# Performance work log

Hardware: AMD Instinct MI355X
Metric: run time of the kernel (lower is better)

Reference implementation:

```python
import jax, jax.numpy as jnp
import numpy as np

B, N, D, K, L, NC = 8, 4096, 64, 8, 2, 2
EPS = 1e-5


def setup_inputs() -> dict:
    key = jax.random.key(0)
    ks = iter(jax.random.split(key, 64))
    def p(*shape, s=0.05):
        return jax.random.normal(next(ks), shape, dtype=jnp.float32) * s
    return dict(
        x=p(B, N, 3, s=1.0),
        ew1=p(3, D), eb1=jnp.zeros((D,), jnp.float32), ew2=p(D, D), eb2=jnp.zeros((D,), jnp.float32),
        wq=p(L, D, D), bq=jnp.zeros((L, D), jnp.float32), wk=p(L, D, D), bk=jnp.zeros((L, D), jnp.float32),
        wv=p(L, D, D), bv=jnp.zeros((L, D), jnp.float32),
        pw1=p(L, 3, D), pb1=jnp.zeros((L, D), jnp.float32), pw2=p(L, D, D), pb2=jnp.zeros((L, D), jnp.float32),
        aw=p(L, D), ab=jnp.zeros((L,), jnp.float32),
        ow=p(L, D, D), ob=jnp.zeros((L, D), jnp.float32),
        l1g=jnp.ones((L, D), jnp.float32), l1b=jnp.zeros((L, D), jnp.float32),
        l2g=jnp.ones((L, D), jnp.float32), l2b=jnp.zeros((L, D), jnp.float32),
        fw1=p(L, D, 2 * D), fb1=jnp.zeros((L, 2 * D), jnp.float32),
        fw2=p(L, 2 * D, D), fb2=jnp.zeros((L, D), jnp.float32),
        cw=p(D, 2 * D), cb=jnp.zeros((2 * D,), jnp.float32),
        cg=jnp.ones((2 * D,), jnp.float32), cbeta=jnp.zeros((2 * D,), jnp.float32),
        f1w=p(2 * D, 128), f1b=jnp.zeros((128,), jnp.float32),
        b1g=jnp.ones((128,), jnp.float32), b1b=jnp.zeros((128,), jnp.float32),
        f2w=p(128, 64), f2b=jnp.zeros((64,), jnp.float32),
        b2g=jnp.ones((64,), jnp.float32), b2b=jnp.zeros((64,), jnp.float32),
        f3w=p(64, NC), f3b=jnp.zeros((NC,), jnp.float32),
    )


def _ln(x, g, b):
    m = jnp.mean(x, -1, keepdims=True)
    v = jnp.mean((x - m) ** 2, -1, keepdims=True)
    return g * (x - m) * jax.lax.rsqrt(v + EPS) + b


def _bn(x, g, b):
    # eval-mode BatchNorm with running_mean=0, running_var=1
    return g * x * jax.lax.rsqrt(jnp.float32(1.0 + EPS)) + b


def _knn(pos, k):
    sq = jnp.sum(pos * pos, -1)  # [B,N]
    d2 = sq[:, :, None] - 2.0 * jnp.einsum('bnd,bmd->bnm', pos, pos) + sq[:, None, :]
    _, idx = jax.lax.top_k(-d2, k)  # k smallest distances (includes self)
    return jax.lax.stop_gradient(idx)  # [B,N,k]


def _gather(t, idx):
    b, n, k = idx.shape
    flat = idx.reshape(b, n * k)
    return jnp.take_along_axis(t, flat[:, :, None], axis=1).reshape(b, n, k, t.shape[-1])


def _block(x, pos, idx, pr):
    (wq, bq, wk, bk, wv, bv, pw1, pb1, pw2, pb2, aw, ab,
     ow, ob, l1g, l1b, l2g, l2b, fw1, fb1, fw2, fb2) = pr
    q = x @ wq + bq
    k = x @ wk + bk
    v = x @ wv + bv
    kg = _gather(k, idx)      # [B,N,K,C]
    vg = _gather(v, idx)
    pg = _gather(pos, idx)    # [B,N,K,3]
    pd = pos[:, :, None, :] - pg
    pe = jax.nn.relu(pd @ pw1 + pb1) @ pw2 + pb2
    ai = q[:, :, None, :] - kg + pe  # subtraction attention
    logits = jnp.einsum('bnkc,c->bnk', ai, aw) + ab
    w = jax.nn.softmax(logits, axis=-1)
    out = jnp.einsum('bnk,bnkc->bnc', w, vg + pe)
    out = out @ ow + ob
    out = _ln(out + x, l1g, l1b)
    ffn = jax.nn.gelu(out @ fw1 + fb1, approximate=False) @ fw2 + fb2
    return _ln(out + ffn, l2g, l2b)


def reference(x, ew1, eb1, ew2, eb2, wq, bq, wk, bk, wv, bv, pw1, pb1, pw2, pb2,
              aw, ab, ow, ob, l1g, l1b, l2g, l2b, fw1, fb1, fw2, fb2,
              cw, cb, cg, cbeta, f1w, f1b, b1g, b1b, f2w, f2b, b2g, b2b, f3w, f3b):
    pos = x
    h = jax.nn.relu(x @ ew1 + eb1) @ ew2 + eb2  # [B,N,D]
    idx = _knn(pos, K)
    stacked = (wq, bq, wk, bk, wv, bv, pw1, pb1, pw2, pb2, aw, ab,
               ow, ob, l1g, l1b, l2g, l2b, fw1, fb1, fw2, fb2)
    for i in range(L):
        h = _block(h, pos, idx, tuple(a[i] for a in stacked))
    y = jax.nn.relu(_bn(h @ cw + cb, cg, cbeta))  # [B,N,2D]
    g = jnp.max(y, axis=1)  # global max pool over points
    g = jax.nn.relu(_bn(g @ f1w + f1b, b1g, b1b))
    g = jax.nn.relu(_bn(g @ f2w + f2b, b2g, b2b))
    return g @ f3w + f3b  # [B, NC]
```

## Files before the change

### kernel.cpp

```cpp
#include <hip/hip_runtime.h>
#include <cmath>

#define BB 8
#define NN 4096
#define DD 64
#define KK 8
#define NCLS 2

constexpr float LNEPS = 1e-5f;
constexpr float BNRS = 0.9999950000374994f;
constexpr float INVSQRT2 = 0.70710678118654752440f;

#define QPB 64
#define SPLITS 16
#define SUBSET 64

__device__ __forceinline__ float wave_sum(float v) {
#pragma unroll
  for (int m = 32; m > 0; m >>= 1) v += __shfl_xor(v, m, 64);
  return v;
}

__device__ __forceinline__ float gelu_exact(float x) {
  return 0.5f * x * (1.0f + erff(x * INVSQRT2));
}

__device__ __forceinline__ float dist2(float4 q, float4 p) {
  float dot = fmaf(q.x, p.x, fmaf(q.y, p.y, q.z * p.z));
  return fmaf(-2.0f, dot, q.w + p.w);
}

__global__ void zero_kernel(float* g) { g[threadIdx.x] = 0.0f; }

__global__ __launch_bounds__(256) void embed_kernel(
    const float* __restrict__ x, const float* __restrict__ ew1, const float* __restrict__ eb1,
    const float* __restrict__ ew2, const float* __restrict__ eb2, float* __restrict__ h) {
  __shared__ float h1[4][DD];
  int w = threadIdx.x >> 6, c = threadIdx.x & 63;
  int pt = ((blockIdx.x & 7) << 12) + (blockIdx.x >> 3) * 4 + w;
  const float* xp = x + (size_t)pt * 3;
  float x0 = xp[0], x1 = xp[1], x2 = xp[2];
  float a = fmaf(x0, ew1[c], fmaf(x1, ew1[64 + c], fmaf(x2, ew1[128 + c], eb1[c])));
  h1[w][c] = fmaxf(a, 0.0f);
  float s = eb2[c];
#pragma unroll 8
  for (int d = 0; d < DD; d++) s = fmaf(h1[w][d], ew2[d * 64 + c], s);
  h[(size_t)pt * 64 + c] = s;
}

__global__ __launch_bounds__(256) void knn_prep_kernel(const float* __restrict__ x,
                                                       float4* __restrict__ ppg) {
  int i = ((blockIdx.x & 7) << 12) + (blockIdx.x >> 3) * 256 + threadIdx.x;
  float a0 = x[3 * i + 0], a1 = x[3 * i + 1], a2 = x[3 * i + 2];
  ppg[i] = make_float4(a0, a1, a2, a0 * a0 + a1 * a1 + a2 * a2);
}

__global__ __launch_bounds__(1024) void knn_kernel(const float4* __restrict__ ppg,
                                                   int* __restrict__ idx) {
  __shared__ union {
    float v[SPLITS * 8][QPB];
    double k[SPLITS * 8][QPB];
  } mb;
  __shared__ float thrq[QPB];
  int b = blockIdx.x & 7;
  int qbase = (blockIdx.x >> 3) * QPB;
  const float4* pb = ppg + (size_t)b * NN;
  int ql = threadIdx.x & 63;
  int sp = __builtin_amdgcn_readfirstlane(threadIdx.x >> 6);
  float4 qp = pb[qbase + ql];
  const float4* cp = pb + sp * (NN / SPLITS);

  float bd[8];
#pragma unroll
  for (int u = 0; u < 8; u++) bd[u] = INFINITY;
#pragma unroll 4
  for (int jj = 0; jj < SUBSET; ++jj) {
    float d2 = dist2(qp, cp[jj]);
#pragma unroll
    for (int u = 7; u > 0; --u) bd[u] = fminf(bd[u], fmaxf(bd[u - 1], d2));
    bd[0] = fminf(bd[0], d2);
  }
#pragma unroll
  for (int u = 0; u < 8; u++) mb.v[sp * 8 + u][ql] = bd[u];
  __syncthreads();

  if (sp < 8) {
    float cd[8];
#pragma unroll
    for (int u = 0; u < 8; u++) cd[u] = INFINITY;
    int base = sp * 16;
#pragma unroll
    for (int e = 0; e < 16; e++) {
      float vv = mb.v[base + e][ql];
#pragma unroll
      for (int u = 7; u > 0; --u) cd[u] = fminf(cd[u], fmaxf(cd[u - 1], vv));
      cd[0] = fminf(cd[0], vv);
    }
#pragma unroll
    for (int u = 0; u < 8; u++) mb.v[base + u][ql] = cd[u];
  }
  __syncthreads();

  if (sp == 0) {
    float cd[8];
#pragma unroll
    for (int u = 0; u < 8; u++) cd[u] = INFINITY;
    for (int m = 0; m < 8; m++) {
      for (int e = 0; e < 8; e++) {
        float vv = mb.v[m * 16 + e][ql];
        if (__all(vv >= cd[7])) break;
#pragma unroll
        for (int u = 7; u > 0; --u) cd[u] = fminf(cd[u], fmaxf(cd[u - 1], vv));
        cd[0] = fminf(cd[0], vv);
      }
    }
    thrq[ql] = cd[7];
  }
  __syncthreads();
  float U = thrq[ql];

  double kd[8];
#pragma unroll
  for (int u = 0; u < 8; u++) kd[u] = INFINITY;
#pragma unroll 4
  for (int jj = 0; jj < NN / SPLITS; ++jj) {
    float d2 = dist2(qp, cp[jj]);
    if (d2 <= U) {
      double key = __hiloint2double(__float_as_int(d2), sp * (NN / SPLITS) + jj);
      if (key < kd[7]) {
#pragma unroll
        for (int u = 7; u > 0; --u) kd[u] = fmin(kd[u], fmax(kd[u - 1], key));
        kd[0] = fmin(kd[0], key);
      }
    }
  }
#pragma unroll
  for (int u = 0; u < 8; u++) mb.k[sp * 8 + u][ql] = kd[u];
  __syncthreads();

  if (sp < 8) {
    double cd[8];
#pragma unroll
    for (int u = 0; u < 8; u++) cd[u] = INFINITY;
    int base = sp * 16;
#pragma unroll
    for (int e = 0; e < 16; e++) {
      double key = mb.k[base + e][ql];
#pragma unroll
      for (int u = 7; u > 0; --u) cd[u] = fmin(cd[u], fmax(cd[u - 1], key));
      cd[0] = fmin(cd[0], key);
    }
#pragma unroll
    for (int u = 0; u < 8; u++) mb.k[base + u][ql] = cd[u];
  }
  __syncthreads();

  if (sp == 0) {
    double cd[8];
#pragma unroll
    for (int u = 0; u < 8; u++) cd[u] = INFINITY;
    for (int m = 0; m < 8; m++) {
      for (int e = 0; e < 8; e++) {
        double key = mb.k[m * 16 + e][ql];
        if (__all(key >= cd[7])) break;
#pragma unroll
        for (int u = 7; u > 0; --u) cd[u] = fmin(cd[u], fmax(cd[u - 1], key));
        cd[0] = fmin(cd[0], key);
      }
    }
    int* op = idx + ((size_t)b * NN + qbase + ql) * 8;
#pragma unroll
    for (int u = 0; u < 8; u++) op[u] = __double2loint(cd[u]);
  }
}

__global__ __launch_bounds__(64) void qkv_kernel(
    const float* __restrict__ h, const float* __restrict__ wq, const float* __restrict__ bq,
    const float* __restrict__ wk, const float* __restrict__ bk,
    const float* __restrict__ wv, const float* __restrict__ bv,
    float* __restrict__ q, float* __restrict__ k, float* __restrict__ v) {
  __shared__ __attribute__((aligned(16))) float hb[DD][4];
  int c = threadIdx.x;
  int b = blockIdx.x & 7, pos = blockIdx.x >> 3;
  int p0 = (b << 12) + pos * 4;
#pragma unroll
  for (int i = 0; i < 4; i++) hb[c][i] = h[(size_t)(p0 + i) * 64 + c];
  float bqc = bq[c], bkc = bk[c], bvc = bv[c];
  float aq[4], ak[4], av[4];
#pragma unroll
  for (int i = 0; i < 4; i++) { aq[i] = bqc; ak[i] = bkc; av[i] = bvc; }
#pragma unroll 4
  for (int d = 0; d < DD; d++) {
    float wq_ = wq[d * 64 + c], wk_ = wk[d * 64 + c], wv_ = wv[d * 64 + c];
    float4 hh = *(const float4*)&hb[d][0];
    aq[0] = fmaf(hh.x, wq_, aq[0]); aq[1] = fmaf(hh.y, wq_, aq[1]);
    aq[2] = fmaf(hh.z, wq_, aq[2]); aq[3] = fmaf(hh.w, wq_, aq[3]);
    ak[0] = fmaf(hh.x, wk_, ak[0]); ak[1] = fmaf(hh.y, wk_, ak[1]);
    ak[2] = fmaf(hh.z, wk_, ak[2]); ak[3] = fmaf(hh.w, wk_, ak[3]);
    av[0] = fmaf(hh.x, wv_, av[0]); av[1] = fmaf(hh.y, wv_, av[1]);
    av[2] = fmaf(hh.z, wv_, av[2]); av[3] = fmaf(hh.w, wv_, av[3]);
  }
#pragma unroll
  for (int i = 0; i < 4; i++) {
    q[(size_t)(p0 + i) * 64 + c] = aq[i];
    k[(size_t)(p0 + i) * 64 + c] = ak[i];
    v[(size_t)(p0 + i) * 64 + c] = av[i];
  }
}

__global__ __launch_bounds__(64) void attn_kernel(
    const float* __restrict__ x, const float* __restrict__ h,
    const float* q, const float* __restrict__ kk, const float* __restrict__ vv,
    const int* __restrict__ idx,
    const float* __restrict__ pw1, const float* __restrict__ pb1,
    const float* __restrict__ pw2, const float* __restrict__ pb2,
    const float* __restrict__ aw, const float* __restrict__ ab,
    const float* __restrict__ ow, const float* __restrict__ ob,
    const float* __restrict__ l1g, const float* __restrict__ l1b,
    float* t) {
  __shared__ __attribute__((aligned(16))) float h1b[2][DD][8];
  __shared__ __attribute__((aligned(16))) float outb[2][DD];
  int c = threadIdx.x;
  int b = blockIdx.x & 7;
  int n0 = (blockIdx.x >> 3) * 2;
  int p0 = (b << 12) + n0;
  const float* xb = x + (size_t)b * NN * 3;
  float w1c0 = pw1[c], w1c1 = pw1[64 + c], w1c2 = pw1[128 + c], b1c = pb1[c];
  float pb2c = pb2[c], lawc = aw[c], lobc = ob[c], g1c = l1g[c], bt1c = l1b[c];
  float lab = ab[0];
  float hs0 = h[(size_t)p0 * 64 + c], hs1 = h[(size_t)(p0 + 1) * 64 + c];
  float qs0 = q[(size_t)p0 * 64 + c], qs1 = q[(size_t)(p0 + 1) * 64 + c];
  int nb[2][8];
#pragma unroll
  for (int u = 0; u < 8; u++) {
    nb[0][u] = idx[(size_t)p0 * 8 + u];
    nb[1][u] = idx[(size_t)(p0 + 1) * 8 + u];
  }
  float kv0[8], kv1[8], vg0[8], vg1[8];
#pragma unroll
  for (int u = 0; u < 8; u++) {
    kv0[u] = kk[((size_t)(b << 12) + nb[0][u]) * 64 + c];
    kv1[u] = kk[((size_t)(b << 12) + nb[1][u]) * 64 + c];
    vg0[u] = vv[((size_t)(b << 12) + nb[0][u]) * 64 + c];
    vg1[u] = vv[((size_t)(b << 12) + nb[1][u]) * 64 + c];
  }
#pragma unroll
  for (int pt = 0; pt < 2; ++pt) {
    int n = n0 + pt;
    float px0 = xb[n * 3 + 0], px1 = xb[n * 3 + 1], px2 = xb[n * 3 + 2];
    float h1v[8];
#pragma unroll
    for (int u = 0; u < 8; u++) {
      int m = nb[pt][u];
      float d0 = px0 - xb[m * 3 + 0], d1 = px1 - xb[m * 3 + 1], d2 = px2 - xb[m * 3 + 2];
      h1v[u] = fmaxf(fmaf(d0, w1c0, fmaf(d1, w1c1, fmaf(d2, w1c2, b1c))), 0.0f);
    }
    *(float4*)&h1b[pt][c][0] = make_float4(h1v[0], h1v[1], h1v[2], h1v[3]);
    *(float4*)&h1b[pt][c][4] = make_float4(h1v[4], h1v[5], h1v[6], h1v[7]);
  }
  float acc0[8], acc1[8];
#pragma unroll
  for (int u = 0; u < 8; u++) { acc0[u] = pb2c; acc1[u] = pb2c; }
#pragma unroll 2
  for (int d = 0; d < DD; d++) {
    float wv_ = pw2[d * 64 + c];
    float4 a0 = *(const float4*)&h1b[0][d][0];
    float4 b0 = *(const float4*)&h1b[0][d][4];
    float4 a1 = *(const float4*)&h1b[1][d][0];
    float4 b1 = *(const float4*)&h1b[1][d][4];
    acc0[0] = fmaf(a0.x, wv_, acc0[0]); acc0[1] = fmaf(a0.y, wv_, acc0[1]);
    acc0[2] = fmaf(a0.z, wv_, acc0[2]); acc0[3] = fmaf(a0.w, wv_, acc0[3]);
    acc0[4] = fmaf(b0.x, wv_, acc0[4]); acc0[5] = fmaf(b0.y, wv_, acc0[5]);
    acc0[6] = fmaf(b0.z, wv_, acc0[6]); acc0[7] = fmaf(b0.w, wv_, acc0[7]);
    acc1[0] = fmaf(a1.x, wv_, acc1[0]); acc1[1] = fmaf(a1.y, wv_, acc1[1]);
    acc1[2] = fmaf(a1.z, wv_, acc1[2]); acc1[3] = fmaf(a1.w, wv_, acc1[3]);
    acc1[4] = fmaf(b1.x, wv_, acc1[4]); acc1[5] = fmaf(b1.y, wv_, acc1[5]);
    acc1[6] = fmaf(b1.z, wv_, acc1[6]); acc1[7] = fmaf(b1.w, wv_, acc1[7]);
  }
  float lg0[8], lg1[8];
#pragma unroll
  for (int u = 0; u < 8; u++) {
    lg0[u] = wave_sum((qs0 - kv0[u] + acc0[u]) * lawc) + lab;
    lg1[u] = wave_sum((qs1 - kv1[u] + acc1[u]) * lawc) + lab;
  }
  float mx0 = lg0[0], mx1 = lg1[0];
#pragma unroll
  for (int u = 1; u < 8; u++) { mx0 = fmaxf(mx0, lg0[u]); mx1 = fmaxf(mx1, lg1[u]); }
  float s0 = 0.0f, s1 = 0.0f;
#pragma unroll
  for (int u = 0; u < 8; u++) {
    lg0[u] = expf(lg0[u] - mx0); s0 += lg0[u];
    lg1[u] = expf(lg1[u] - mx1); s1 += lg1[u];
  }
  float i0 = 1.0f / s0, i1 = 1.0f / s1;
  float out0 = 0.0f, out1 = 0.0f;
#pragma unroll
  for (int u = 0; u < 8; u++) {
    out0 = fmaf(lg0[u] * i0, vg0[u] + acc0[u], out0);
    out1 = fmaf(lg1[u] * i1, vg1[u] + acc1[u], out1);
  }
  outb[0][c] = out0; outb[1][c] = out1;
  float at0 = lobc, at1 = lobc;
#pragma unroll 4
  for (int d = 0; d < DD; d += 4) {
    float4 o0 = *(const float4*)&outb[0][d];
    float4 o1 = *(const float4*)&outb[1][d];
    float wa = ow[(d + 0) * 64 + c], wb = ow[(d + 1) * 64 + c];
    float wc = ow[(d + 2) * 64 + c], wd = ow[(d + 3) * 64 + c];
    at0 = fmaf(o0.x, wa, at0); at0 = fmaf(o0.y, wb, at0);
    at0 = fmaf(o0.z, wc, at0); at0 = fmaf(o0.w, wd, at0);
    at1 = fmaf(o1.x, wa, at1); at1 = fmaf(o1.y, wb, at1);
    at1 = fmaf(o1.z, wc, at1); at1 = fmaf(o1.w, wd, at1);
  }
  {
    float res = at0 + hs0;
    float mean = wave_sum(res) * (1.0f / 64.0f);
    float dv = res - mean;
    float var = wave_sum(dv * dv) * (1.0f / 64.0f);
    float ivr = 1.0f / sqrtf(var + LNEPS);
    t[(size_t)p0 * 64 + c] = fmaf(g1c, dv * ivr, bt1c);
  }
  {
    float res = at1 + hs1;
    float mean = wave_sum(res) * (1.0f / 64.0f);
    float dv = res - mean;
    float var = wave_sum(dv * dv) * (1.0f / 64.0f);
    float ivr = 1.0f / sqrtf(var + LNEPS);
    t[(size_t)(p0 + 1) * 64 + c] = fmaf(g1c, dv * ivr, bt1c);
  }
}

__global__ __launch_bounds__(64) void ffn_kernel(
    const float* __restrict__ t, const float* __restrict__ fw1, const float* __restrict__ fb1,
    const float* __restrict__ fw2, const float* __restrict__ fb2,
    const float* __restrict__ l2g, const float* __restrict__ l2b, float* __restrict__ h) {
  __shared__ __attribute__((aligned(16))) float yb[DD][4];
  __shared__ __attribute__((aligned(16))) float hb[128][4];
  int c = threadIdx.x;
  int b = blockIdx.x & 7, pos = blockIdx.x >> 3;
  int p0 = (b << 12) + pos * 4;
  float y[4];
#pragma unroll
  for (int i = 0; i < 4; i++) { y[i] = t[(size_t)(p0 + i) * 64 + c]; yb[c][i] = y[i]; }
  float b1a = fb1[c], b1b = fb1[64 + c];
  float b2c = fb2[c], g2c = l2g[c], bt2c = l2b[c];
  float hA[4], hB[4];
#pragma unroll
  for (int i = 0; i < 4; i++) { hA[i] = b1a; hB[i] = b1b; }
#pragma unroll 4
  for (int d = 0; d < DD; d++) {
    float w0 = fw1[d * 128 + c], w1 = fw1[d * 128 + 64 + c];
    float4 yv = *(const float4*)&yb[d][0];
    hA[0] = fmaf(yv.x, w0, hA[0]); hA[1] = fmaf(yv.y, w0, hA[1]);
    hA[2] = fmaf(yv.z, w0, hA[2]); hA[3] = fmaf(yv.w, w0, hA[3]);
    hB[0] = fmaf(yv.x, w1, hB[0]); hB[1] = fmaf(yv.y, w1, hB[1]);
    hB[2] = fmaf(yv.z, w1, hB[2]); hB[3] = fmaf(yv.w, w1, hB[3]);
  }
#pragma unroll
  for (int i = 0; i < 4; i++) {
    hA[i] = gelu_exact(hA[i]); hB[i] = gelu_exact(hB[i]);
    hb[c][i] = hA[i]; hb[64 + c][i] = hB[i];
  }
  float o[4];
#pragma unroll
  for (int i = 0; i < 4; i++) o[i] = b2c;
#pragma unroll 4
  for (int j = 0; j < 128; j++) {
    float wv_ = fw2[j * 64 + c];
    float4 hv = *(const float4*)&hb[j][0];
    o[0] = fmaf(hv.x, wv_, o[0]); o[1] = fmaf(hv.y, wv_, o[1]);
    o[2] = fmaf(hv.z, wv_, o[2]); o[3] = fmaf(hv.w, wv_, o[3]);
  }
#pragma unroll
  for (int i = 0; i < 4; i++) {
    float r = y[i] + o[i];
    float mean = wave_sum(r) * (1.0f / 64.0f);
    float dv = r - mean;
    float var = wave_sum(dv * dv) * (1.0f / 64.0f);
    float ivr = 1.0f / sqrtf(var + LNEPS);
    h[(size_t)(p0 + i) * 64 + c] = fmaf(g2c, dv * ivr, bt2c);
  }
}

__global__ __launch_bounds__(256) void cls_kernel(
    const float* __restrict__ h, const float* __restrict__ cw, const float* __restrict__ cb,
    const float* __restrict__ cg, const float* __restrict__ cbeta, float* __restrict__ g) {
  __shared__ float lcw[DD * 128];
  __shared__ float lcb[128], lcg[128], lcbt[128];
  __shared__ __attribute__((aligned(16))) float hb[4][DD][4];
  __shared__ float wmax[4][128];
  int tid = threadIdx.x;
  for (int i = tid; i < DD * 128; i += 256) lcw[i] = cw[i];
  if (tid < 128) { lcb[tid] = cb[tid]; lcg[tid] = cg[tid]; lcbt[tid] = cbeta[tid]; }
  __syncthreads();
  int w = tid >> 6, c = tid & 63;
  int b = blockIdx.x & 7;
  int blk = blockIdx.x >> 3;
  int base = b * NN + blk * 32;
  float m0 = 0.0f, m1 = 0.0f;
  for (int it = 0; it < 2; ++it) {
    int p0 = base + (w * 2 + it) * 4;
#pragma unroll
    for (int i = 0; i < 4; i++) hb[w][c][i] = h[(size_t)(p0 + i) * 64 + c];
    float a0[4], a1[4];
#pragma unroll
    for (int i = 0; i < 4; i++) { a0[i] = lcb[c]; a1[i] = lcb[64 + c]; }
#pragma unroll 4
    for (int d = 0; d < DD; d++) {
      float w0 = lcw[d * 128 + c], w1 = lcw[d * 128 + 64 + c];
      float4 hv = *(const float4*)&hb[w][d][0];
      a0[0] = fmaf(hv.x, w0, a0[0]); a0[1] = fmaf(hv.y, w0, a0[1]);
      a0[2] = fmaf(hv.z, w0, a0[2]); a0[3] = fmaf(hv.w, w0, a0[3]);
      a1[0] = fmaf(hv.x, w1, a1[0]); a1[1] = fmaf(hv.y, w1, a1[1]);
      a1[2] = fmaf(hv.z, w1, a1[2]); a1[3] = fmaf(hv.w, w1, a1[3]);
    }
#pragma unroll
    for (int i = 0; i < 4; i++) {
      m0 = fmaxf(m0, fmaxf(0.0f, fmaf(lcg[c] * a0[i], BNRS, lcbt[c])));
      m1 = fmaxf(m1, fmaxf(0.0f, fmaf(lcg[64 + c] * a1[i], BNRS, lcbt[64 + c])));
    }
  }
  wmax[w][c] = m0; wmax[w][64 + c] = m1;
  __syncthreads();
  if (tid < 128) {
    float mm = fmaxf(fmaxf(wmax[0][tid], wmax[1][tid]), fmaxf(wmax[2][tid], wmax[3][tid]));
    atomicMax((int*)&g[b * 128 + tid], __float_as_int(mm));
  }
}

__global__ __launch_bounds__(128) void head_kernel(
    const float* __restrict__ g,
    const float* __restrict__ f1w, const float* __restrict__ f1b,
    const float* __restrict__ b1g, const float* __restrict__ b1b,
    const float* __restrict__ f2w, const float* __restrict__ f2b,
    const float* __restrict__ b2g, const float* __restrict__ b2b,
    const float* __restrict__ f3w, const float* __restrict__ f3b,
    float* __restrict__ out) {
  __shared__ float gb[128], g1[128], g2[64];
  int b = blockIdx.x, t = threadIdx.x;
  gb[t] = g[b * 128 + t];
  __syncthreads();
  float a = f1b[t];
#pragma unroll 4
  for (int d = 0; d < 128; d++) a = fmaf(gb[d], f1w[d * 128 + t], a);
  g1[t] = fmaxf(0.0f, fmaf(b1g[t] * a, BNRS, b1b[t]));
  __syncthreads();
  if (t < 64) {
    float a2 = f2b[t];
#pragma unroll 4
    for (int j = 0; j < 128; j++) a2 = fmaf(g1[j], f2w[j * 64 + t], a2);
    g2[t] = fmaxf(0.0f, fmaf(b2g[t] * a2, BNRS, b2b[t]));
  }
  __syncthreads();
  if (t < NCLS) {
    float a3 = f3b[t];
#pragma unroll
    for (int d = 0; d < 64; d++) a3 = fmaf(g2[d], f3w[d * NCLS + t], a3);
    out[b * NCLS + t] = a3;
  }
}

extern "C" void kernel_launch(void* const* d_in, const int* in_sizes, int n_in,
                              void* d_out, int out_size, void* d_ws, size_t ws_size,
                              hipStream_t stream) {
  const float* x    = (const float*)d_in[0];
  const float* ew1  = (const float*)d_in[1];
  const float* eb1  = (const float*)d_in[2];
  const float* ew2  = (const float*)d_in[3];
  const float* eb2  = (const float*)d_in[4];
  const float* wq   = (const float*)d_in[5];
  const float* bq   = (const float*)d_in[6];
  const float* wk   = (const float*)d_in[7];
  const float* bk   = (const float*)d_in[8];
  const float* wv   = (const float*)d_in[9];
  const float* bv   = (const float*)d_in[10];
  const float* pw1  = (const float*)d_in[11];
  const float* pb1  = (const float*)d_in[12];
  const float* pw2  = (const float*)d_in[13];
  const float* pb2  = (const float*)d_in[14];
  const float* aw   = (const float*)d_in[15];
  const float* ab   = (const float*)d_in[16];
  const float* ow   = (const float*)d_in[17];
  const float* ob   = (const float*)d_in[18];
  const float* l1g  = (const float*)d_in[19];
  const float* l1b  = (const float*)d_in[20];
  const float* l2g  = (const float*)d_in[21];
  const float* l2b  = (const float*)d_in[22];
  const float* fw1  = (const float*)d_in[23];
  const float* fb1  = (const float*)d_in[24];
  const float* fw2  = (const float*)d_in[25];
  const float* fb2  = (const float*)d_in[26];
  const float* cw   = (const float*)d_in[27];
  const float* cb   = (const float*)d_in[28];
  const float* cg   = (const float*)d_in[29];
  const float* cbeta= (const float*)d_in[30];
  const float* f1w  = (const float*)d_in[31];
  const float* f1b  = (const float*)d_in[32];
  const float* b1g  = (const float*)d_in[33];
  const float* b1b  = (const float*)d_in[34];
  const float* f2w  = (const float*)d_in[35];
  const float* f2b  = (const float*)d_in[36];
  const float* b2g  = (const float*)d_in[37];
  const float* b2b  = (const float*)d_in[38];
  const float* f3w  = (const float*)d_in[39];
  const float* f3b  = (const float*)d_in[40];

  const size_t P = (size_t)BB * NN;
  float* ws = (float*)d_ws;
  float* h = ws;
  float* q = h + P * 64;
  float* k = q + P * 64;
  float* v = k + P * 64;
  int* idx = (int*)(v + P * 64);
  float* g = (float*)(idx + P * 8);
  float4* ppg = (float4*)(g + BB * 128);
  float* t = q;

  zero_kernel<<<1, BB * 128, 0, stream>>>(g);
  embed_kernel<<<(int)(P / 4), 256, 0, stream>>>(x, ew1, eb1, ew2, eb2, h);
  knn_prep_kernel<<<(int)(P / 256), 256, 0, stream>>>(x, ppg);
  knn_kernel<<<BB * (NN / QPB), 1024, 0, stream>>>(ppg, idx);
  for (int l = 0; l < 2; l++) {
    qkv_kernel<<<(int)(P / 4), 64, 0, stream>>>(h, wq + l * DD * DD, bq + l * DD,
                                                wk + l * DD * DD, bk + l * DD,
                                                wv + l * DD * DD, bv + l * DD, q, k, v);
    attn_kernel<<<(int)(P / 2), 64, 0, stream>>>(x, h, q, k, v, idx,
                                                 pw1 + l * 3 * DD, pb1 + l * DD,
                                                 pw2 + l * DD * DD, pb2 + l * DD,
                                                 aw + l * DD, ab + l,
                                                 ow + l * DD * DD, ob + l * DD,
                                                 l1g + l * DD, l1b + l * DD, t);
    ffn_kernel<<<(int)(P / 4), 64, 0, stream>>>(t, fw1 + l * DD * 2 * DD, fb1 + l * 2 * DD,
                                                fw2 + l * 2 * DD * DD, fb2 + l * DD,
                                                l2g + l * DD, l2b + l * DD, h);
  }
  cls_kernel<<<BB * 128, 256, 0, stream>>>(h, cw, cb, cg, cbeta, g);
  head_kernel<<<BB, 128, 0, stream>>>(g, f1w, f1b, b1g, b1b, f2w, f2b, b2g, b2b, f3w, f3b,
                                      (float*)d_out);
}
```

Before: 372.8 us.

## Fuse attention and FFN kernels; use shared-memory replace-max for KNN candidates

The attention and FFN stages become one kernel. The first layernorm output stays in registers and LDS instead of going through a global scratch buffer, which also saves a launch per layer. The FFN part now handles 2 points per block instead of 4, so each weight load is reused across fewer points. Separately, the per-split KNN top-8 moves from a sorted register insertion network of doubles to an unsorted LDS array with a linear max-replace scan. This is meant to cut register pressure, but it adds LDS traffic and divergent branches per accepted candidate.

```diff
diff --git a/kernel.cpp b/kernel.cpp
--- a/kernel.cpp
+++ b/kernel.cpp
@@ -119,23 +119,30 @@
   __syncthreads();
   float U = thrq[ql];
 
-  double kd[8];
-#pragma unroll
-  for (int u = 0; u < 8; u++) kd[u] = INFINITY;
+#pragma unroll
+  for (int u = 0; u < 8; u++) mb.k[sp * 8 + u][ql] = INFINITY;
+
+  int cnt = 0;
 #pragma unroll 4
   for (int jj = 0; jj < NN / SPLITS; ++jj) {
     float d2 = dist2(qp, cp[jj]);
     if (d2 <= U) {
       double key = __hiloint2double(__float_as_int(d2), sp * (NN / SPLITS) + jj);
-      if (key < kd[7]) {
-#pragma unroll
-        for (int u = 7; u > 0; --u) kd[u] = fmin(kd[u], fmax(kd[u - 1], key));
-        kd[0] = fmin(kd[0], key);
+      if (cnt < 8) {
+        mb.k[sp * 8 + cnt][ql] = key;
+        cnt++;
+      } else {
+        double mx = mb.k[sp * 8 + 0][ql];
+        int mi = 0;
+#pragma unroll
+        for (int u = 1; u < 8; u++) {
+          double tv = mb.k[sp * 8 + u][ql];
+          if (tv > mx) { mx = tv; mi = u; }
+        }
+        if (key < mx) mb.k[sp * 8 + mi][ql] = key;
       }
     }
   }
-#pragma unroll
-  for (int u = 0; u < 8; u++) mb.k[sp * 8 + u][ql] = kd[u];
   __syncthreads();
 
   if (sp < 8) {
@@ -208,18 +215,22 @@
   }
 }
 
-__global__ __launch_bounds__(64) void attn_kernel(
-    const float* __restrict__ x, const float* __restrict__ h,
-    const float* q, const float* __restrict__ kk, const float* __restrict__ vv,
+__global__ __launch_bounds__(64) void attn_ffn_kernel(
+    const float* __restrict__ x, float* h,
+    const float* __restrict__ q, const float* __restrict__ kk, const float* __restrict__ vv,
     const int* __restrict__ idx,
     const float* __restrict__ pw1, const float* __restrict__ pb1,
     const float* __restrict__ pw2, const float* __restrict__ pb2,
     const float* __restrict__ aw, const float* __restrict__ ab,
     const float* __restrict__ ow, const float* __restrict__ ob,
     const float* __restrict__ l1g, const float* __restrict__ l1b,
-    float* t) {
+    const float* __restrict__ fw1, const float* __restrict__ fb1,
+    const float* __restrict__ fw2, const float* __restrict__ fb2,
+    const float* __restrict__ l2g, const float* __restrict__ l2b) {
   __shared__ __attribute__((aligned(16))) float h1b[2][DD][8];
   __shared__ __attribute__((aligned(16))) float outb[2][DD];
+  __shared__ __attribute__((aligned(8)))  float tb[DD][2];
+  __shared__ __attribute__((aligned(8)))  float hb2[128][2];
   int c = threadIdx.x;
   int b = blockIdx.x & 7;
   int n0 = (blockIdx.x >> 3) * 2;
@@ -312,13 +323,14 @@
     at1 = fmaf(o1.x, wa, at1); at1 = fmaf(o1.y, wb, at1);
     at1 = fmaf(o1.z, wc, at1); at1 = fmaf(o1.w, wd, at1);
   }
+  float t0v, t1v;
   {
     float res = at0 + hs0;
     float mean = wave_sum(res) * (1.0f / 64.0f);
     float dv = res - mean;
     float var = wave_sum(dv * dv) * (1.0f / 64.0f);
     float ivr = 1.0f / sqrtf(var + LNEPS);
-    t[(size_t)p0 * 64 + c] = fmaf(g1c, dv * ivr, bt1c);
+    t0v = fmaf(g1c, dv * ivr, bt1c);
   }
   {
     float res = at1 + hs1;
@@ -326,59 +338,45 @@
     float dv = res - mean;
     float var = wave_sum(dv * dv) * (1.0f / 64.0f);
     float ivr = 1.0f / sqrtf(var + LNEPS);
-    t[(size_t)(p0 + 1) * 64 + c] = fmaf(g1c, dv * ivr, bt1c);
-  }
-}
-
-__global__ __launch_bounds__(64) void ffn_kernel(
-    const float* __restrict__ t, const float* __restrict__ fw1, const float* __restrict__ fb1,
-    const float* __restrict__ fw2, const float* __restrict__ fb2,
-    const float* __restrict__ l2g, const float* __restrict__ l2b, float* __restrict__ h) {
-  __shared__ __attribute__((aligned(16))) float yb[DD][4];
-  __shared__ __attribute__((aligned(16))) float hb[128][4];
-  int c = threadIdx.x;
-  int b = blockIdx.x & 7, pos = blockIdx.x >> 3;
-  int p0 = (b << 12) + pos * 4;
-  float y[4];
-#pragma unroll
-  for (int i = 0; i < 4; i++) { y[i] = t[(size_t)(p0 + i) * 64 + c]; yb[c][i] = y[i]; }
-  float b1a = fb1[c], b1b = fb1[64 + c];
-  float b2c = fb2[c], g2c = l2g[c], bt2c = l2b[c];
-  float hA[4], hB[4];
-#pragma unroll
-  for (int i = 0; i < 4; i++) { hA[i] = b1a; hB[i] = b1b; }
+    t1v = fmaf(g1c, dv * ivr, bt1c);
+  }
+  tb[c][0] = t0v; tb[c][1] = t1v;
+  float fb1a = fb1[c], fb1b = fb1[64 + c];
+  float hA0 = fb1a, hA1 = fb1a, hB0 = fb1b, hB1 = fb1b;
 #pragma unroll 4
   for (int d = 0; d < DD; d++) {
     float w0 = fw1[d * 128 + c], w1 = fw1[d * 128 + 64 + c];
-    float4 yv = *(const float4*)&yb[d][0];
-    hA[0] = fmaf(yv.x, w0, hA[0]); hA[1] = fmaf(yv.y, w0, hA[1]);
-    hA[2] = fmaf(yv.z, w0, hA[2]); hA[3] = fmaf(yv.w, w0, hA[3]);
-    hB[0] = fmaf(yv.x, w1, hB[0]); hB[1] = fmaf(yv.y, w1, hB[1]);
-    hB[2] = fmaf(yv.z, w1, hB[2]); hB[3] = fmaf(yv.w, w1, hB[3]);
-  }
-#pragma unroll
-  for (int i = 0; i < 4; i++) {
-    hA[i] = gelu_exact(hA[i]); hB[i] = gelu_exact(hB[i]);
-    hb[c][i] = hA[i]; hb[64 + c][i] = hB[i];
-  }
-  float o[4];
-#pragma unroll
-  for (int i = 0; i < 4; i++) o[i] = b2c;
+    float2 yv = *(const float2*)&tb[d][0];
+    hA0 = fmaf(yv.x, w0, hA0); hA1 = fmaf(yv.y, w0, hA1);
+    hB0 = fmaf(yv.x, w1, hB0); hB1 = fmaf(yv.y, w1, hB1);
+  }
+  hA0 = gelu_exact(hA0); hA1 = gelu_exact(hA1);
+  hB0 = gelu_exact(hB0); hB1 = gelu_exact(hB1);
+  hb2[c][0] = hA0; hb2[c][1] = hA1;
+  hb2[64 + c][0] = hB0; hb2[64 + c][1] = hB1;
+  float fb2c = fb2[c], g2c = l2g[c], bt2c = l2b[c];
+  float o0 = fb2c, o1 = fb2c;
 #pragma unroll 4
   for (int j = 0; j < 128; j++) {
     float wv_ = fw2[j * 64 + c];
-    float4 hv = *(const float4*)&hb[j][0];
-    o[0] = fmaf(hv.x, wv_, o[0]); o[1] = fmaf(hv.y, wv_, o[1]);
-    o[2] = fmaf(hv.z, wv_, o[2]); o[3] = fmaf(hv.w, wv_, o[3]);
-  }
-#pragma unroll
-  for (int i = 0; i < 4; i++) {
-    float r = y[i] + o[i];
+    float2 hv = *(const float2*)&hb2[j][0];
+    o0 = fmaf(hv.x, wv_, o0); o1 = fmaf(hv.y, wv_, o1);
+  }
+  {
+    float r = t0v + o0;
     float mean = wave_sum(r) * (1.0f / 64.0f);
     float dv = r - mean;
     float var = wave_sum(dv * dv) * (1.0f / 64.0f);
     float ivr = 1.0f / sqrtf(var + LNEPS);
-    h[(size_t)(p0 + i) * 64 + c] = fmaf(g2c, dv * ivr, bt2c);
+    h[(size_t)p0 * 64 + c] = fmaf(g2c, dv * ivr, bt2c);
+  }
+  {
+    float r = t1v + o1;
+    float mean = wave_sum(r) * (1.0f / 64.0f);
+    float dv = r - mean;
+    float var = wave_sum(dv * dv) * (1.0f / 64.0f);
+    float ivr = 1.0f / sqrtf(var + LNEPS);
+    h[(size_t)(p0 + 1) * 64 + c] = fmaf(g2c, dv * ivr, bt2c);
   }
 }
 
@@ -514,7 +512,6 @@
   int* idx = (int*)(v + P * 64);
   float* g = (float*)(idx + P * 8);
   float4* ppg = (float4*)(g + BB * 128);
-  float* t = q;
 
   zero_kernel<<<1, BB * 128, 0, stream>>>(g);
   embed_kernel<<<(int)(P / 4), 256, 0, stream>>>(x, ew1, eb1, ew2, eb2, h);
@@ -524,15 +521,13 @@
     qkv_kernel<<<(int)(P / 4), 64, 0, stream>>>(h, wq + l * DD * DD, bq + l * DD,
                                                 wk + l * DD * DD, bk + l * DD,
                                                 wv + l * DD * DD, bv + l * DD, q, k, v);
-    attn_kernel<<<(int)(P / 2), 64, 0, stream>>>(x, h, q, k, v, idx,
-                                                 pw1 + l * 3 * DD, pb1 + l * DD,
-                                                 pw2 + l * DD * DD, pb2 + l * DD,
-                                                 aw + l * DD, ab + l,
-                                                 ow + l * DD * DD, ob + l * DD,
-                                                 l1g + l * DD, l1b + l * DD, t);
-    ffn_kernel<<<(int)(P / 4), 64, 0, stream>>>(t, fw1 + l * DD * 2 * DD, fb1 + l * 2 * DD,
-                                                fw2 + l * 2 * DD * DD, fb2 + l * DD,
-                                                l2g + l * DD, l2b + l * DD, h);
+    attn_ffn_kernel<<<(int)(P / 2), 64, 0, stream>>>(
+        x, h, q, k, v, idx,
+        pw1 + l * 3 * DD, pb1 + l * DD, pw2 + l * DD * DD, pb2 + l * DD,
+        aw + l * DD, ab + l, ow + l * DD * DD, ob + l * DD,
+        l1g + l * DD, l1b + l * DD,
+        fw1 + l * DD * 2 * DD, fb1 + l * 2 * DD, fw2 + l * 2 * DD * DD, fb2 + l * DD,
+        l2g + l * DD, l2b + l * DD);
   }
   cls_kernel<<<BB * 128, 256, 0, stream>>>(h, cw, cb, cg, cbeta, g);
   head_kernel<<<BB, 128, 0, stream>>>(g, f1w, f1b, b1g, b1b, f2w, f2b, b2g, b2b, f3w, f3b,
```

Result: no change. 366.6 us (median of 2 runs) (-1.6%).
